# Optimization experiments

Hardware: AMD Instinct MI355X
Metric: run time of the kernel (lower is better)

## Reference

```python
import jax, jax.numpy as jnp
import numpy as np

N = 10000
E = 640000
F = 128      # in_dim
H = 4        # heads
Dh = 32      # head_dim = ceil(128/4)
INNER = H * Dh   # 128 == out_dim -> W_out is Identity
OUT = 128
SCALE = 1.0 / np.sqrt(float(Dh))
LN_EPS = 1e-5


def setup_inputs() -> dict:
    key = jax.random.key(0)
    ks = jax.random.split(key, 8)
    s = 1.0 / np.sqrt(F)
    nodes = jax.random.normal(ks[0], (N, F), dtype=jnp.float32)
    edge_index = jax.random.randint(ks[1], (2, E), 0, N, dtype=jnp.int32)
    W_Q = jax.random.uniform(ks[2], (F, INNER), jnp.float32, -s, s)
    W_K = jax.random.uniform(ks[3], (F, INNER), jnp.float32, -s, s)
    W_V = jax.random.uniform(ks[4], (F, INNER), jnp.float32, -s, s)
    W_res = jax.random.uniform(ks[5], (F, OUT), jnp.float32, -s, s)
    b_res = jax.random.uniform(ks[6], (OUT,), jnp.float32, -s, s)
    gamma = jnp.ones((OUT,), jnp.float32)
    beta = jnp.zeros((OUT,), jnp.float32)
    return {"nodes": nodes, "W_Q": W_Q, "W_K": W_K, "W_V": W_V,
            "W_res": W_res, "b_res": b_res, "gamma": gamma, "beta": beta,
            "edge_index": edge_index}


def reference(nodes, W_Q, W_K, W_V, W_res, b_res, gamma, beta, edge_index):
    n = nodes.shape[0]
    src = edge_index[0]
    dst = edge_index[1]
    # node-level projections, split into heads: [N, H, Dh]
    Q = (nodes @ W_Q).reshape(n, H, Dh)
    K = (nodes @ W_K).reshape(n, H, Dh)
    V = (nodes @ W_V).reshape(n, H, Dh)
    # per-edge gathers: q from dst, k/v from src
    q = Q[dst]          # [E, H, Dh]
    k = K[src]
    v = V[src]
    score = jnp.sum(q * k, axis=-1) * SCALE      # [E, H]
    # segment softmax over dst
    mx = jax.ops.segment_max(score, dst, num_segments=n)   # [N, H]
    mx = jnp.where(jnp.isfinite(mx), mx, 0.0)               # guard empty segments
    ex = jnp.exp(score - mx[dst])                           # [E, H]
    sm = jax.ops.segment_sum(ex, dst, num_segments=n)       # [N, H]
    alpha = ex / (sm[dst] + 1e-12)                          # [E, H]
    # scatter-aggregate weighted values
    agg = jax.ops.segment_sum(alpha[:, :, None] * v, dst, num_segments=n)  # [N, H, Dh]
    H_cat = agg.reshape(n, INNER)                # W_out is Identity (inner == out)
    H_out = H_cat + nodes @ W_res + b_res        # residual projection
    # LayerNorm(out_dim)
    mu = jnp.mean(H_out, axis=-1, keepdims=True)
    var = jnp.mean(jnp.square(H_out - mu), axis=-1, keepdims=True)
    x_hat = (H_out - mu) * jax.lax.rsqrt(var + LN_EPS)
    return gamma * x_hat + beta
```

## Files before the change

kernel.cpp:

```cpp
#include <hip/hip_runtime.h>
#include <math.h>

#define FDIM 128
#define NP 64
#define NMAX 10240
static constexpr float SC2 = 0.17677669529663687f * 1.4426950408889634f;
static constexpr float LN_EPS = 1e-5f;

typedef __attribute__((ext_vector_type(8))) short bf16x8;
typedef __attribute__((ext_vector_type(4))) float f32x4;

__device__ __forceinline__ unsigned short f2bf(float f) {
    unsigned u = __float_as_uint(f);
    unsigned r = u + 0x7FFFu + ((u >> 16) & 1u);
    return (unsigned short)(r >> 16);
}

__global__ __launch_bounds__(256) void prep_kernel(
    const float* __restrict__ Wq, const float* __restrict__ Wk,
    const float* __restrict__ Wv, const float* __restrict__ Wr,
    unsigned short* __restrict__ Wt)
{
    const int tid = threadIdx.x;
    const int t = blockIdx.x;
    const int wiW = t >> 2, q = t & 3;
    const float* __restrict__ W = (wiW == 0) ? Wq : (wiW == 1) ? Wk : (wiW == 2) ? Wv : Wr;
    const int c = q * 32 + (tid >> 3);
    const int k0 = (tid & 7) * 16;
    unsigned short* dp = &Wt[(size_t)wiW * 16384 + c * 128 + k0];
    #pragma unroll
    for (int kk = 0; kk < 16; ++kk)
        dp[kk] = f2bf(W[(k0 + kk) * FDIM + c]);
}

__global__ __launch_bounds__(256) void gemm_hist_kernel(
    const float* __restrict__ nodes,
    const unsigned short* __restrict__ Wt,
    const float* __restrict__ br,
    unsigned short* __restrict__ Qu, unsigned short* __restrict__ KVu,
    float* __restrict__ Rb, int N,
    const int* __restrict__ dst, int* __restrict__ bh,
    int* __restrict__ rank, int E, int C)
{
    __shared__ __align__(16) char smem[52224];
    const int tid = threadIdx.x;
    const int wi = blockIdx.y;

    if (wi == 0) {
        const int p = blockIdx.x;
        if (p >= NP) return;
        int* h = (int*)smem;
        for (int i = tid; i < N; i += 256) h[i] = 0;
        __syncthreads();
        const int lo = p * C;
        const int hi = min(lo + C, E);
        const int n = hi - lo;
        if (n > 0) {
            if (((lo | E) & 3) == 0) {
                const int4* d4 = (const int4*)(dst + lo);
                int4* r4p = (int4*)(rank + lo);
                const int n4 = n >> 2;
                for (int i = tid; i < n4; i += 256) {
                    int4 d = d4[i];
                    int4 r;
                    r.x = atomicAdd(&h[d.x], 1);
                    r.y = atomicAdd(&h[d.y], 1);
                    r.z = atomicAdd(&h[d.z], 1);
                    r.w = atomicAdd(&h[d.w], 1);
                    r4p[i] = r;
                }
                for (int i = lo + (n4 << 2) + tid; i < hi; i += 256)
                    rank[i] = atomicAdd(&h[dst[i]], 1);
            } else {
                for (int i = lo + tid; i < hi; i += 256)
                    rank[i] = atomicAdd(&h[dst[i]], 1);
            }
        }
        __syncthreads();
        for (int i = tid; i < N; i += 256) bh[p * N + i] = h[i];
        return;
    }

    const int gw = wi - 1;
    const int row0 = blockIdx.x * 64;
    unsigned short (*As)[136] = (unsigned short(*)[136])smem;
    unsigned short (*Ws)[136] = (unsigned short(*)[136])(smem + 64 * 272);

    #pragma unroll
    for (int i = 0; i < 8; ++i) {
        const int idx = tid + i * 256;
        const int r = idx >> 5, c4 = idx & 31;
        const int gr = row0 + r;
        float4 v = make_float4(0.f, 0.f, 0.f, 0.f);
        if (gr < N) v = *reinterpret_cast<const float4*>(&nodes[(size_t)gr * FDIM + c4 * 4]);
        ushort4 o;
        o.x = f2bf(v.x); o.y = f2bf(v.y); o.z = f2bf(v.z); o.w = f2bf(v.w);
        *reinterpret_cast<ushort4*>(&As[r][c4 * 4]) = o;
    }
    const unsigned short* Wg = &Wt[(size_t)gw * 16384];
    #pragma unroll
    for (int i = 0; i < 8; ++i) {
        const int idx = tid + i * 256;
        const int r = idx >> 4, ch = idx & 15;
        const uint4 v = *reinterpret_cast<const uint4*>(&Wg[r * 128 + ch * 8]);
        *reinterpret_cast<uint4*>(&Ws[r][ch * 8]) = v;
    }
    __syncthreads();

    const int w = tid >> 6;
    const int l = tid & 63;
    const int lr = l & 15;
    const int lh = l >> 4;

    f32x4 acc[8];
    #pragma unroll
    for (int ct = 0; ct < 8; ++ct) acc[ct] = (f32x4){0.f, 0.f, 0.f, 0.f};

    #pragma unroll
    for (int kc = 0; kc < 4; ++kc) {
        const bf16x8 a = *reinterpret_cast<const bf16x8*>(&As[w * 16 + lr][kc * 32 + lh * 8]);
        #pragma unroll
        for (int ct = 0; ct < 8; ++ct) {
            const bf16x8 bb = *reinterpret_cast<const bf16x8*>(&Ws[ct * 16 + lr][kc * 32 + lh * 8]);
            acc[ct] = __builtin_amdgcn_mfma_f32_16x16x32_bf16(a, bb, acc[ct], 0, 0, 0);
        }
    }

    const int rbase = row0 + w * 16 + lh * 4;
    #pragma unroll
    for (int ct = 0; ct < 8; ++ct) {
        const int col = ct * 16 + lr;
        float bc = 0.f;
        if (gw == 3) bc = br[col];
        #pragma unroll
        for (int r = 0; r < 4; ++r) {
            const int row = rbase + r;
            if (row >= N) continue;
            const float val = acc[ct][r];
            if (gw == 0)      Qu[(size_t)row * 128 + col] = f2bf(val);
            else if (gw == 1) KVu[(size_t)row * 256 + col] = f2bf(val);
            else if (gw == 2) KVu[(size_t)row * 256 + 128 + col] = f2bf(val);
            else              Rb[(size_t)row * 128 + col] = val + bc;
        }
    }
}

__global__ __launch_bounds__(256) void degrel_kernel(
    int* __restrict__ bh, int* __restrict__ deg, int N)
{
    const int d = blockIdx.x * 256 + threadIdx.x;
    if (d < N) {
        int c = 0;
        #pragma unroll
        for (int p = 0; p < NP; ++p) {
            const int cnt = bh[p * N + d];
            bh[p * N + d] = c;
            c += cnt;
        }
        deg[d] = c;
    }
}

__global__ __launch_bounds__(1024) void scan_kernel(
    const int* __restrict__ deg, int* __restrict__ rowptr, int N)
{
    __shared__ int tot[NMAX];
    __shared__ int wsum[16];
    const int tid = threadIdx.x;
    const int lane = tid & 63;
    const int wid = tid >> 6;

    for (int d = tid; d < N; d += 1024) tot[d] = deg[d];
    __syncthreads();

    const int CH = (N + 1023) / 1024;
    const int b = tid * CH;
    const int e = min(b + CH, N);
    int s = 0;
    for (int i = b; i < e; ++i) s += tot[i];

    int incl = s;
    #pragma unroll
    for (int off = 1; off < 64; off <<= 1) {
        int t = __shfl_up(incl, off);
        if (lane >= off) incl += t;
    }
    if (lane == 63) wsum[wid] = incl;
    __syncthreads();
    if (wid == 0) {
        int v = (lane < 16) ? wsum[lane] : 0;
        #pragma unroll
        for (int off = 1; off < 16; off <<= 1) {
            int t = __shfl_up(v, off);
            if (lane >= off) v += t;
        }
        if (lane < 16) wsum[lane] = v;
    }
    __syncthreads();
    const int wbase = (wid > 0) ? wsum[wid - 1] : 0;
    int run = wbase + incl - s;
    for (int i = b; i < e; ++i) {
        const int t = tot[i];
        rowptr[i] = run;
        run += t;
    }
    if (tid == 1023) rowptr[N] = wsum[15];
}

__global__ __launch_bounds__(256) void scatter_kernel(
    const int* __restrict__ src, const int* __restrict__ dst,
    const int* __restrict__ rank, const int* __restrict__ rel,
    const int* __restrict__ rowptr, int* __restrict__ ssrc,
    int N, int E, int C)
{
    const int p = blockIdx.x >> 3;
    const int sub = blockIdx.x & 7;
    const int CS = C >> 3;
    const int lo = p * C + sub * CS;
    const int hi = min(lo + CS, E);
    const int n = hi - lo;
    if (n <= 0) return;
    const int* rp = &rel[p * N];

    if (((lo | E) & 3) == 0) {
        const int4* s4 = (const int4*)(src + lo);
        const int4* d4 = (const int4*)(dst + lo);
        const int4* r4 = (const int4*)(rank + lo);
        const int n4 = n >> 2;
        for (int i = threadIdx.x; i < n4; i += 256) {
            const int4 s = s4[i];
            const int4 d = d4[i];
            const int4 r = r4[i];
            ssrc[rowptr[d.x] + rp[d.x] + r.x] = s.x;
            ssrc[rowptr[d.y] + rp[d.y] + r.y] = s.y;
            ssrc[rowptr[d.z] + rp[d.z] + r.z] = s.z;
            ssrc[rowptr[d.w] + rp[d.w] + r.w] = s.w;
        }
        for (int i = lo + (n4 << 2) + threadIdx.x; i < hi; i += 256)
            ssrc[rowptr[dst[i]] + rp[dst[i]] + rank[i]] = src[i];
    } else {
        for (int i = lo + threadIdx.x; i < hi; i += 256)
            ssrc[rowptr[dst[i]] + rp[dst[i]] + rank[i]] = src[i];
    }
}

__global__ __launch_bounds__(256) void agg_kernel(
    const unsigned short* __restrict__ Qu, const unsigned short* __restrict__ KVu,
    const float* __restrict__ Rb,
    const int* __restrict__ rowptr, const int* __restrict__ ssrc,
    const float* __restrict__ gamma, const float* __restrict__ beta,
    float* __restrict__ out, int N)
{
    __shared__ float sA[8][16][8];
    __shared__ float sL[8][16];

    const int wave = threadIdx.x >> 6;
    const int lane = threadIdx.x & 63;
    const int qtr = lane >> 4;
    const int lq = lane & 15;
    const int slot = wave * 2 + (qtr >> 1);
    const int s = qtr & 1;
    const int n = blockIdx.x * 8 + slot;
    const bool active = (n < N);
    const int d0 = lq * 8;

    uint4 qu = make_uint4(0u, 0u, 0u, 0u);
    int beg = 0, end = 0;
    if (active) {
        qu = *reinterpret_cast<const uint4*>(&Qu[(size_t)n * 128 + d0]);
        beg = rowptr[n];
        end = rowptr[n + 1];
    }
    const float qf0 = __uint_as_float(qu.x << 16), qf1 = __uint_as_float(qu.x & 0xFFFF0000u);
    const float qf2 = __uint_as_float(qu.y << 16), qf3 = __uint_as_float(qu.y & 0xFFFF0000u);
    const float qf4 = __uint_as_float(qu.z << 16), qf5 = __uint_as_float(qu.z & 0xFFFF0000u);
    const float qf6 = __uint_as_float(qu.w << 16), qf7 = __uint_as_float(qu.w & 0xFFFF0000u);

    const int nbAll = (end - beg) >> 2;
    const int nbh = (nbAll + 1) >> 1;
    const int b0 = (s == 0) ? 0 : nbh;
    const int b1 = (s == 0) ? nbh : nbAll;
    const int j0 = beg + b0 * 4;
    const int m = b1 - b0;

    float4 A0a = make_float4(0.f, 0.f, 0.f, 0.f), A0b = A0a;
    float4 A1a = A0a, A1b = A0a, A2a = A0a, A2b = A0a, A3a = A0a, A3b = A0a;
    float L0 = 0.f, L1 = 0.f, L2 = 0.f, L3 = 0.f;

#define GATHER(S, NK, NV)                                                     \
    {                                                                         \
        const unsigned short* bp = &KVu[(size_t)(S) * 256 + d0];              \
        NK = *reinterpret_cast<const uint4*>(bp);                             \
        NV = *reinterpret_cast<const uint4*>(bp + 128);                       \
    }
#define STEP(KU, VU, Aa, Ab, L)                                               \
    {                                                                         \
        const float k0 = __uint_as_float((KU).x << 16), k1 = __uint_as_float((KU).x & 0xFFFF0000u); \
        const float k2 = __uint_as_float((KU).y << 16), k3 = __uint_as_float((KU).y & 0xFFFF0000u); \
        const float k4 = __uint_as_float((KU).z << 16), k5 = __uint_as_float((KU).z & 0xFFFF0000u); \
        const float k6 = __uint_as_float((KU).w << 16), k7 = __uint_as_float((KU).w & 0xFFFF0000u); \
        float p = qf0 * k0 + qf1 * k1 + qf2 * k2 + qf3 * k3                   \
                + qf4 * k4 + qf5 * k5 + qf6 * k6 + qf7 * k7;                  \
        p += __shfl_xor(p, 1);                                                \
        p += __shfl_xor(p, 2);                                                \
        const float e1 = exp2f(p * SC2);                                      \
        const float v0 = __uint_as_float((VU).x << 16), v1 = __uint_as_float((VU).x & 0xFFFF0000u); \
        const float v2 = __uint_as_float((VU).y << 16), v3 = __uint_as_float((VU).y & 0xFFFF0000u); \
        const float v4 = __uint_as_float((VU).z << 16), v5 = __uint_as_float((VU).z & 0xFFFF0000u); \
        const float v6 = __uint_as_float((VU).w << 16), v7 = __uint_as_float((VU).w & 0xFFFF0000u); \
        Aa.x += e1 * v0; Aa.y += e1 * v1; Aa.z += e1 * v2; Aa.w += e1 * v3;   \
        Ab.x += e1 * v4; Ab.y += e1 * v5; Ab.z += e1 * v6; Ab.w += e1 * v7;   \
        L += e1;                                                              \
    }

    uint4 nk0, nv0, nk1, nv1, nk2, nv2, nk3, nv3;
    if (m > 0) {
        int c0i = ssrc[j0], c1i = ssrc[j0 + 1], c2i = ssrc[j0 + 2], c3i = ssrc[j0 + 3];
        GATHER(c0i, nk0, nv0); GATHER(c1i, nk1, nv1);
        GATHER(c2i, nk2, nv2); GATHER(c3i, nk3, nv3);
        int x0 = ssrc[j0 + 4], x1 = ssrc[j0 + 5], x2 = ssrc[j0 + 6], x3 = ssrc[j0 + 7];
        for (int bi = 1; bi < m; ++bi) {
            const uint4 ck0 = nk0, cv0 = nv0, ck1 = nk1, cv1 = nv1;
            const uint4 ck2 = nk2, cv2 = nv2, ck3 = nk3, cv3 = nv3;
            c0i = x0; c1i = x1; c2i = x2; c3i = x3;
            const int nbase = j0 + (bi + 1) * 4;
            x0 = ssrc[nbase]; x1 = ssrc[nbase + 1];
            x2 = ssrc[nbase + 2]; x3 = ssrc[nbase + 3];
            GATHER(c0i, nk0, nv0); GATHER(c1i, nk1, nv1);
            GATHER(c2i, nk2, nv2); GATHER(c3i, nk3, nv3);
            STEP(ck0, cv0, A0a, A0b, L0);
            STEP(ck1, cv1, A1a, A1b, L1);
            STEP(ck2, cv2, A2a, A2b, L2);
            STEP(ck3, cv3, A3a, A3b, L3);
        }
        STEP(nk0, nv0, A0a, A0b, L0);
        STEP(nk1, nv1, A1a, A1b, L1);
        STEP(nk2, nv2, A2a, A2b, L2);
        STEP(nk3, nv3, A3a, A3b, L3);
    }
    if (s == 1) {
        for (int j = beg + nbAll * 4; j < end; ++j) {
            const int s0 = ssrc[j];
            uint4 k0u, v0u;
            GATHER(s0, k0u, v0u);
            STEP(k0u, v0u, A0a, A0b, L0);
        }
    }
#undef GATHER
#undef STEP

    float a0 = (A0a.x + A1a.x) + (A2a.x + A3a.x);
    float a1 = (A0a.y + A1a.y) + (A2a.y + A3a.y);
    float a2 = (A0a.z + A1a.z) + (A2a.z + A3a.z);
    float a3 = (A0a.w + A1a.w) + (A2a.w + A3a.w);
    float a4 = (A0b.x + A1b.x) + (A2b.x + A3b.x);
    float a5 = (A0b.y + A1b.y) + (A2b.y + A3b.y);
    float a6 = (A0b.z + A1b.z) + (A2b.z + A3b.z);
    float a7 = (A0b.w + A1b.w) + (A2b.w + A3b.w);
    float L = (L0 + L1) + (L2 + L3);

    if (s == 1) {
        float* dp = &sA[slot][lq][0];
        dp[0] = a0; dp[1] = a1; dp[2] = a2; dp[3] = a3;
        dp[4] = a4; dp[5] = a5; dp[6] = a6; dp[7] = a7;
        sL[slot][lq] = L;
    }
    __syncthreads();
    if (s == 1 || !active) return;

    {
        const float* dp = &sA[slot][lq][0];
        a0 += dp[0]; a1 += dp[1]; a2 += dp[2]; a3 += dp[3];
        a4 += dp[4]; a5 += dp[5]; a6 += dp[6]; a7 += dp[7];
        L += sL[slot][lq];
    }

    const float inv = 1.f / (L + 1e-12f);
    const float4 ra = *reinterpret_cast<const float4*>(&Rb[(size_t)n * 128 + d0]);
    const float4 rb = *reinterpret_cast<const float4*>(&Rb[(size_t)n * 128 + d0 + 4]);
    float xa0 = a0 * inv + ra.x;
    float xa1 = a1 * inv + ra.y;
    float xa2 = a2 * inv + ra.z;
    float xa3 = a3 * inv + ra.w;
    float xb0 = a4 * inv + rb.x;
    float xb1 = a5 * inv + rb.y;
    float xb2 = a6 * inv + rb.z;
    float xb3 = a7 * inv + rb.w;

    float s1v = (xa0 + xa1 + xa2 + xa3) + (xb0 + xb1 + xb2 + xb3);
    float s2v = xa0 * xa0 + xa1 * xa1 + xa2 * xa2 + xa3 * xa3
              + xb0 * xb0 + xb1 * xb1 + xb2 * xb2 + xb3 * xb3;
    #pragma unroll
    for (int off = 8; off; off >>= 1) {
        s1v += __shfl_xor(s1v, off);
        s2v += __shfl_xor(s2v, off);
    }
    const float mu = s1v * (1.f / 128.f);
    float var = s2v * (1.f / 128.f) - mu * mu;
    var = fmaxf(var, 0.f);
    const float rs = rsqrtf(var + LN_EPS);

    const float4 ga = *reinterpret_cast<const float4*>(&gamma[d0]);
    const float4 gb = *reinterpret_cast<const float4*>(&gamma[d0 + 4]);
    const float4 ba = *reinterpret_cast<const float4*>(&beta[d0]);
    const float4 bb = *reinterpret_cast<const float4*>(&beta[d0 + 4]);
    float4 oa, ob;
    oa.x = ga.x * (xa0 - mu) * rs + ba.x;
    oa.y = ga.y * (xa1 - mu) * rs + ba.y;
    oa.z = ga.z * (xa2 - mu) * rs + ba.z;
    oa.w = ga.w * (xa3 - mu) * rs + ba.w;
    ob.x = gb.x * (xb0 - mu) * rs + bb.x;
    ob.y = gb.y * (xb1 - mu) * rs + bb.y;
    ob.z = gb.z * (xb2 - mu) * rs + bb.z;
    ob.w = gb.w * (xb3 - mu) * rs + bb.w;
    *reinterpret_cast<float4*>(&out[(size_t)n * 128 + d0]) = oa;
    *reinterpret_cast<float4*>(&out[(size_t)n * 128 + d0 + 4]) = ob;
}

extern "C" void kernel_launch(void* const* d_in, const int* in_sizes, int n_in,
                              void* d_out, int out_size, void* d_ws, size_t ws_size,
                              hipStream_t stream)
{
    const float* nodes = (const float*)d_in[0];
    const float* W_Q   = (const float*)d_in[1];
    const float* W_K   = (const float*)d_in[2];
    const float* W_V   = (const float*)d_in[3];
    const float* W_res = (const float*)d_in[4];
    const float* b_res = (const float*)d_in[5];
    const float* gamma = (const float*)d_in[6];
    const float* beta  = (const float*)d_in[7];
    const int*   eidx  = (const int*)d_in[8];

    const int N = in_sizes[0] / FDIM;
    const int E = in_sizes[8] / 2;
    const int* src = eidx;
    const int* dst = eidx + E;

    float* out = (float*)d_out;

    unsigned short* KVu = (unsigned short*)d_ws;
    unsigned short* Qu  = KVu + (size_t)N * 256;
    unsigned short* Wt  = Qu + (size_t)N * 128;
    float* Rb   = (float*)(Wt + 4 * 16384);
    int* bh     = (int*)(Rb + (size_t)N * 128);
    int* rowptr = bh + (size_t)NP * N;
    int* deg    = rowptr + (N + 1);
    int* rank   = deg + N;
    int* ssrc   = rank + E;

    const int C = (((E + NP - 1) / NP) + 31) & ~31;
    const int nG = (N + 63) / 64;
    const int nB = (N + 255) / 256;

    prep_kernel<<<16, 256, 0, stream>>>(W_Q, W_K, W_V, W_res, Wt);

    dim3 ggrid(nG, 5);
    gemm_hist_kernel<<<ggrid, 256, 0, stream>>>(nodes, Wt, b_res,
                                                Qu, KVu, Rb, N, dst, bh, rank, E, C);
    degrel_kernel<<<nB, 256, 0, stream>>>(bh, deg, N);
    scan_kernel<<<1, 1024, 0, stream>>>(deg, rowptr, N);
    scatter_kernel<<<NP * 8, 256, 0, stream>>>(src, dst, rank, bh, rowptr, ssrc, N, E, C);
    agg_kernel<<<(N + 7) / 8, 256, 0, stream>>>(Qu, KVu, Rb, rowptr, ssrc,
                                                gamma, beta, out, N);
}
```

Measured before the change: 89.34 us.

## Regroup preprocessing stages to cut kernel launches and overlap GEMM with scatter

Merges weight conversion with the destination histogram into one launch. The degree prefix is merged with the scan, using a last-block-done atomic counter so the final block computes rowptr. The edge scatter now runs in the same grid as the projection GEMM. This drops from six launches to four and lets scatter traffic overlap GEMM work. In exchange, the scan runs on only 256 threads reading deg from global memory, and the GEMM grid gains idle blocks that exit early.

```diff
diff --git a/kernel.cpp b/kernel.cpp
--- a/kernel.cpp
+++ b/kernel.cpp
@@ -16,71 +16,175 @@
     return (unsigned short)(r >> 16);
 }
 
-__global__ __launch_bounds__(256) void prep_kernel(
+__global__ __launch_bounds__(256) void prep_hist_kernel(
     const float* __restrict__ Wq, const float* __restrict__ Wk,
     const float* __restrict__ Wv, const float* __restrict__ Wr,
-    unsigned short* __restrict__ Wt)
+    unsigned short* __restrict__ Wt,
+    const int* __restrict__ dst, int* __restrict__ bh,
+    int* __restrict__ rank, int* __restrict__ done,
+    int N, int E, int C)
 {
+    __shared__ int h[NMAX];
     const int tid = threadIdx.x;
-    const int t = blockIdx.x;
-    const int wiW = t >> 2, q = t & 3;
-    const float* __restrict__ W = (wiW == 0) ? Wq : (wiW == 1) ? Wk : (wiW == 2) ? Wv : Wr;
-    const int c = q * 32 + (tid >> 3);
-    const int k0 = (tid & 7) * 16;
-    unsigned short* dp = &Wt[(size_t)wiW * 16384 + c * 128 + k0];
-    #pragma unroll
-    for (int kk = 0; kk < 16; ++kk)
-        dp[kk] = f2bf(W[(k0 + kk) * FDIM + c]);
-}
-
-__global__ __launch_bounds__(256) void gemm_hist_kernel(
+    const int b = blockIdx.x;
+
+    if (b < 16) {
+        if (b == 0 && tid == 0) *done = 0;
+        const int wiW = b >> 2, q = b & 3;
+        const float* __restrict__ W = (wiW == 0) ? Wq : (wiW == 1) ? Wk : (wiW == 2) ? Wv : Wr;
+        const int c = q * 32 + (tid >> 3);
+        const int k0 = (tid & 7) * 16;
+        unsigned short* dp = &Wt[(size_t)wiW * 16384 + c * 128 + k0];
+        #pragma unroll
+        for (int kk = 0; kk < 16; ++kk)
+            dp[kk] = f2bf(W[(k0 + kk) * FDIM + c]);
+        return;
+    }
+
+    const int p = b - 16;
+    if (p >= NP) return;
+    for (int i = tid; i < N; i += 256) h[i] = 0;
+    __syncthreads();
+    const int lo = p * C;
+    const int hi = min(lo + C, E);
+    const int n = hi - lo;
+    if (n > 0) {
+        if (((lo | E) & 3) == 0) {
+            const int4* d4 = (const int4*)(dst + lo);
+            int4* r4p = (int4*)(rank + lo);
+            const int n4 = n >> 2;
+            for (int i = tid; i < n4; i += 256) {
+                int4 d = d4[i];
+                int4 r;
+                r.x = atomicAdd(&h[d.x], 1);
+                r.y = atomicAdd(&h[d.y], 1);
+                r.z = atomicAdd(&h[d.z], 1);
+                r.w = atomicAdd(&h[d.w], 1);
+                r4p[i] = r;
+            }
+            for (int i = lo + (n4 << 2) + tid; i < hi; i += 256)
+                rank[i] = atomicAdd(&h[dst[i]], 1);
+        } else {
+            for (int i = lo + tid; i < hi; i += 256)
+                rank[i] = atomicAdd(&h[dst[i]], 1);
+        }
+    }
+    __syncthreads();
+    for (int i = tid; i < N; i += 256) bh[p * N + i] = h[i];
+}
+
+__global__ __launch_bounds__(256) void degrel_scan_kernel(
+    int* __restrict__ bh, int* __restrict__ deg, int* __restrict__ rowptr,
+    int* __restrict__ done, int N)
+{
+    __shared__ int wsum[4];
+    __shared__ int lastFlag;
+    const int tid = threadIdx.x;
+    const int d = blockIdx.x * 256 + tid;
+
+    if (d < N) {
+        int c = 0;
+        #pragma unroll
+        for (int p = 0; p < NP; ++p) {
+            const int cnt = bh[p * N + d];
+            bh[p * N + d] = c;
+            c += cnt;
+        }
+        deg[d] = c;
+    }
+
+    __threadfence();
+    if (tid == 0) {
+        const int old = atomicAdd(done, 1);
+        lastFlag = (old == (int)gridDim.x - 1);
+    }
+    __syncthreads();
+    if (!lastFlag) return;
+    __threadfence();
+
+    const int lane = tid & 63;
+    const int wid = tid >> 6;
+    const int CH = (N + 255) / 256;
+    const int b0 = tid * CH;
+    const int e0 = min(b0 + CH, N);
+    int s = 0;
+    for (int i = b0; i < e0; ++i) s += deg[i];
+
+    int incl = s;
+    #pragma unroll
+    for (int off = 1; off < 64; off <<= 1) {
+        int t = __shfl_up(incl, off);
+        if (lane >= off) incl += t;
+    }
+    if (lane == 63) wsum[wid] = incl;
+    __syncthreads();
+    if (wid == 0) {
+        int v = (lane < 4) ? wsum[lane] : 0;
+        #pragma unroll
+        for (int off = 1; off < 4; off <<= 1) {
+            int t = __shfl_up(v, off);
+            if (lane >= off) v += t;
+        }
+        if (lane < 4) wsum[lane] = v;
+    }
+    __syncthreads();
+    const int wbase = (wid > 0) ? wsum[wid - 1] : 0;
+    int run = wbase + incl - s;
+    for (int i = b0; i < e0; ++i) {
+        rowptr[i] = run;
+        run += deg[i];
+    }
+    if (tid == 255) rowptr[N] = wsum[3];
+}
+
+__global__ __launch_bounds__(256) void gemm_scatter_kernel(
     const float* __restrict__ nodes,
     const unsigned short* __restrict__ Wt,
     const float* __restrict__ br,
     unsigned short* __restrict__ Qu, unsigned short* __restrict__ KVu,
-    float* __restrict__ Rb, int N,
-    const int* __restrict__ dst, int* __restrict__ bh,
-    int* __restrict__ rank, int E, int C)
+    float* __restrict__ Rb, int N, int nG,
+    const int* __restrict__ src, const int* __restrict__ dst,
+    const int* __restrict__ rank, const int* __restrict__ rel,
+    const int* __restrict__ rowptr, int* __restrict__ ssrc, int E, int C)
 {
     __shared__ __align__(16) char smem[52224];
     const int tid = threadIdx.x;
     const int wi = blockIdx.y;
 
     if (wi == 0) {
-        const int p = blockIdx.x;
-        if (p >= NP) return;
-        int* h = (int*)smem;
-        for (int i = tid; i < N; i += 256) h[i] = 0;
-        __syncthreads();
-        const int lo = p * C;
-        const int hi = min(lo + C, E);
+        const int p = blockIdx.x >> 3;
+        const int sub = blockIdx.x & 7;
+        const int CS = C >> 3;
+        const int lo = p * C + sub * CS;
+        const int hi = min(lo + CS, E);
         const int n = hi - lo;
-        if (n > 0) {
-            if (((lo | E) & 3) == 0) {
-                const int4* d4 = (const int4*)(dst + lo);
-                int4* r4p = (int4*)(rank + lo);
-                const int n4 = n >> 2;
-                for (int i = tid; i < n4; i += 256) {
-                    int4 d = d4[i];
-                    int4 r;
-                    r.x = atomicAdd(&h[d.x], 1);
-                    r.y = atomicAdd(&h[d.y], 1);
-                    r.z = atomicAdd(&h[d.z], 1);
-                    r.w = atomicAdd(&h[d.w], 1);
-                    r4p[i] = r;
-                }
-                for (int i = lo + (n4 << 2) + tid; i < hi; i += 256)
-                    rank[i] = atomicAdd(&h[dst[i]], 1);
-            } else {
-                for (int i = lo + tid; i < hi; i += 256)
-                    rank[i] = atomicAdd(&h[dst[i]], 1);
+        if (n <= 0) return;
+        const int* rp = &rel[p * N];
+
+        if (((lo | E) & 3) == 0) {
+            const int4* s4 = (const int4*)(src + lo);
+            const int4* d4 = (const int4*)(dst + lo);
+            const int4* r4 = (const int4*)(rank + lo);
+            const int n4 = n >> 2;
+            for (int i = tid; i < n4; i += 256) {
+                const int4 s = s4[i];
+                const int4 d = d4[i];
+                const int4 r = r4[i];
+                ssrc[rowptr[d.x] + rp[d.x] + r.x] = s.x;
+                ssrc[rowptr[d.y] + rp[d.y] + r.y] = s.y;
+                ssrc[rowptr[d.z] + rp[d.z] + r.z] = s.z;
+                ssrc[rowptr[d.w] + rp[d.w] + r.w] = s.w;
             }
-        }
-        __syncthreads();
-        for (int i = tid; i < N; i += 256) bh[p * N + i] = h[i];
+            for (int i = lo + (n4 << 2) + tid; i < hi; i += 256)
+                ssrc[rowptr[dst[i]] + rp[dst[i]] + rank[i]] = src[i];
+        } else {
+            for (int i = lo + tid; i < hi; i += 256)
+                ssrc[rowptr[dst[i]] + rp[dst[i]] + rank[i]] = src[i];
+        }
         return;
     }
 
+    if ((int)blockIdx.x >= nG) return;
     const int gw = wi - 1;
     const int row0 = blockIdx.x * 64;
     unsigned short (*As)[136] = (unsigned short(*)[136])smem;
@@ -142,105 +246,6 @@
             else if (gw == 2) KVu[(size_t)row * 256 + 128 + col] = f2bf(val);
             else              Rb[(size_t)row * 128 + col] = val + bc;
         }
-    }
-}
-
-__global__ __launch_bounds__(256) void degrel_kernel(
-    int* __restrict__ bh, int* __restrict__ deg, int N)
-{
-    const int d = blockIdx.x * 256 + threadIdx.x;
-    if (d < N) {
-        int c = 0;
-        #pragma unroll
-        for (int p = 0; p < NP; ++p) {
-            const int cnt = bh[p * N + d];
-            bh[p * N + d] = c;
-            c += cnt;
-        }
-        deg[d] = c;
-    }
-}
-
-__global__ __launch_bounds__(1024) void scan_kernel(
-    const int* __restrict__ deg, int* __restrict__ rowptr, int N)
-{
-    __shared__ int tot[NMAX];
-    __shared__ int wsum[16];
-    const int tid = threadIdx.x;
-    const int lane = tid & 63;
-    const int wid = tid >> 6;
-
-    for (int d = tid; d < N; d += 1024) tot[d] = deg[d];
-    __syncthreads();
-
-    const int CH = (N + 1023) / 1024;
-    const int b = tid * CH;
-    const int e = min(b + CH, N);
-    int s = 0;
-    for (int i = b; i < e; ++i) s += tot[i];
-
-    int incl = s;
-    #pragma unroll
-    for (int off = 1; off < 64; off <<= 1) {
-        int t = __shfl_up(incl, off);
-        if (lane >= off) incl += t;
-    }
-    if (lane == 63) wsum[wid] = incl;
-    __syncthreads();
-    if (wid == 0) {
-        int v = (lane < 16) ? wsum[lane] : 0;
-        #pragma unroll
-        for (int off = 1; off < 16; off <<= 1) {
-            int t = __shfl_up(v, off);
-            if (lane >= off) v += t;
-        }
-        if (lane < 16) wsum[lane] = v;
-    }
-    __syncthreads();
-    const int wbase = (wid > 0) ? wsum[wid - 1] : 0;
-    int run = wbase + incl - s;
-    for (int i = b; i < e; ++i) {
-        const int t = tot[i];
-        rowptr[i] = run;
-        run += t;
-    }
-    if (tid == 1023) rowptr[N] = wsum[15];
-}
-
-__global__ __launch_bounds__(256) void scatter_kernel(
-    const int* __restrict__ src, const int* __restrict__ dst,
-    const int* __restrict__ rank, const int* __restrict__ rel,
-    const int* __restrict__ rowptr, int* __restrict__ ssrc,
-    int N, int E, int C)
-{
-    const int p = blockIdx.x >> 3;
-    const int sub = blockIdx.x & 7;
-    const int CS = C >> 3;
-    const int lo = p * C + sub * CS;
-    const int hi = min(lo + CS, E);
-    const int n = hi - lo;
-    if (n <= 0) return;
-    const int* rp = &rel[p * N];
-
-    if (((lo | E) & 3) == 0) {
-        const int4* s4 = (const int4*)(src + lo);
-        const int4* d4 = (const int4*)(dst + lo);
-        const int4* r4 = (const int4*)(rank + lo);
-        const int n4 = n >> 2;
-        for (int i = threadIdx.x; i < n4; i += 256) {
-            const int4 s = s4[i];
-            const int4 d = d4[i];
-            const int4 r = r4[i];
-            ssrc[rowptr[d.x] + rp[d.x] + r.x] = s.x;
-            ssrc[rowptr[d.y] + rp[d.y] + r.y] = s.y;
-            ssrc[rowptr[d.z] + rp[d.z] + r.z] = s.z;
-            ssrc[rowptr[d.w] + rp[d.w] + r.w] = s.w;
-        }
-        for (int i = lo + (n4 << 2) + threadIdx.x; i < hi; i += 256)
-            ssrc[rowptr[dst[i]] + rp[dst[i]] + rank[i]] = src[i];
-    } else {
-        for (int i = lo + threadIdx.x; i < hi; i += 256)
-            ssrc[rowptr[dst[i]] + rp[dst[i]] + rank[i]] = src[i];
     }
 }
 
@@ -447,19 +452,21 @@
     int* deg    = rowptr + (N + 1);
     int* rank   = deg + N;
     int* ssrc   = rank + E;
+    int* done   = ssrc + E + 8;
 
     const int C = (((E + NP - 1) / NP) + 31) & ~31;
     const int nG = (N + 63) / 64;
     const int nB = (N + 255) / 256;
 
-    prep_kernel<<<16, 256, 0, stream>>>(W_Q, W_K, W_V, W_res, Wt);
-
-    dim3 ggrid(nG, 5);
-    gemm_hist_kernel<<<ggrid, 256, 0, stream>>>(nodes, Wt, b_res,
-                                                Qu, KVu, Rb, N, dst, bh, rank, E, C);
-    degrel_kernel<<<nB, 256, 0, stream>>>(bh, deg, N);
-    scan_kernel<<<1, 1024, 0, stream>>>(deg, rowptr, N);
-    scatter_kernel<<<NP * 8, 256, 0, stream>>>(src, dst, rank, bh, rowptr, ssrc, N, E, C);
+    prep_hist_kernel<<<16 + NP, 256, 0, stream>>>(W_Q, W_K, W_V, W_res, Wt,
+                                                  dst, bh, rank, done, N, E, C);
+    degrel_scan_kernel<<<nB, 256, 0, stream>>>(bh, deg, rowptr, done, N);
+
+    dim3 ggrid(NP * 8, 5);
+    gemm_scatter_kernel<<<ggrid, 256, 0, stream>>>(nodes, Wt, b_res,
+                                                   Qu, KVu, Rb, N, nG,
+                                                   src, dst, rank, bh, rowptr,
+                                                   ssrc, E, C);
     agg_kernel<<<(N + 7) / 8, 256, 0, stream>>>(Qu, KVu, Rb, rowptr, ssrc,
                                                 gamma, beta, out, N);
 }
```

Result: slower. 99.84 us (+11.7%).
